# Kernel optimization log

Hardware: AMD Instinct MI355X
Metric: run time of the kernel (lower is better)

## Reference

```python
import jax, jax.numpy as jnp
import numpy as np

B, PIX_H, PIX_W = 64, 14, 14
ENC_D, DEC_D, ATT_D, EMB_D = 2048, 512, 512, 512
VOCAB, MAX_LEN = 10000, 52  # 51 decode steps


def setup_inputs() -> dict:
    key = jax.random.key(0)
    ks = jax.random.split(key, 24)
    s = 0.02
    inp = {
        'encoder_out': jax.random.normal(ks[0], (B, PIX_H, PIX_W, ENC_D), jnp.float32),
        'encoded_captions': jax.random.randint(ks[1], (B, MAX_LEN), 0, VOCAB),
        'caption_lengths': jnp.sort(jax.random.randint(ks[2], (B,), 2, MAX_LEN + 1))[::-1].at[0].set(MAX_LEN),
        # embedding (uniform -0.1..0.1 as in init_weights)
        'emb': jax.random.uniform(ks[3], (VOCAB, EMB_D), jnp.float32, -0.1, 0.1),
        # attention network
        'W_enc_att': jax.random.normal(ks[4], (ENC_D, ATT_D)) * s,
        'b_enc_att': jnp.zeros((ATT_D,)),
        'W_dec_att': jax.random.normal(ks[5], (DEC_D, ATT_D)) * s,
        'b_dec_att': jnp.zeros((ATT_D,)),
        'W_full_att': jax.random.normal(ks[6], (ATT_D, 1)) * s,
        'b_full_att': jnp.zeros((1,)),
        # init hidden state
        'W_init_h': jax.random.normal(ks[7], (ENC_D, DEC_D)) * s,
        'b_init_h': jnp.zeros((DEC_D,)),
        'W_init_c': jax.random.normal(ks[8], (ENC_D, DEC_D)) * s,
        'b_init_c': jnp.zeros((DEC_D,)),
        # gate
        'W_fbeta': jax.random.normal(ks[9], (DEC_D, ENC_D)) * s,
        'b_fbeta': jnp.zeros((ENC_D,)),
        # LSTMCell (torch gate order i,f,g,o)
        'W_ih': jax.random.normal(ks[10], (EMB_D + ENC_D, 4 * DEC_D)) * s,
        'W_hh': jax.random.normal(ks[11], (DEC_D, 4 * DEC_D)) * s,
        'b_ih': jnp.zeros((4 * DEC_D,)),
        'b_hh': jnp.zeros((4 * DEC_D,)),
        # fc (uniform -0.1..0.1, zero bias per init_weights)
        'W_fc': jax.random.uniform(ks[12], (DEC_D, VOCAB), jnp.float32, -0.1, 0.1),
        'b_fc': jnp.zeros((VOCAB,)),
    }
    return inp


def _decode(encoder_out, encoded_captions, caption_lengths, emb,
            W_enc_att, b_enc_att, W_dec_att, b_dec_att, W_full_att, b_full_att,
            W_init_h, b_init_h, W_init_c, b_init_c, W_fbeta, b_fbeta,
            W_ih, W_hh, b_ih, b_hh, W_fc, b_fc):
    bsz = encoder_out.shape[0]
    enc = encoder_out.reshape(bsz, -1, encoder_out.shape[-1])  # [B, P, ENC_D]
    embeddings = emb[encoded_captions]                          # [B, T+1, E]
    mean_enc = enc.mean(axis=1)
    h0 = mean_enc @ W_init_h + b_init_h
    c0 = mean_enc @ W_init_c + b_init_c
    att_enc = enc @ W_enc_att + b_enc_att                       # [B, P, A] precomputed
    T = encoded_captions.shape[1] - 1                           # max decode steps
    decode_len = caption_lengths - 1                            # [B]
    step_mask = jnp.arange(T)[:, None] < decode_len[None, :]    # [T, B]
    emb_seq = jnp.swapaxes(embeddings[:, :T, :], 0, 1)          # [T, B, E]

    def step(carry, xt):
        h, c = carry
        emb_t, m = xt                                           # [B,E], [B]
        # attention: 2 linears + tanh + softmax + weighted sum
        att_dec = h @ W_dec_att + b_dec_att                     # [B, A]
        e = (jnp.tanh(att_enc + att_dec[:, None, :]) @ W_full_att + b_full_att)[..., 0]  # [B, P]
        alpha = jax.nn.softmax(e, axis=-1)
        awe = jnp.einsum('bp,bpd->bd', alpha, enc)              # [B, ENC_D]
        gate = jax.nn.sigmoid(h @ W_fbeta + b_fbeta)
        awe = gate * awe
        # LSTMCell
        x = jnp.concatenate([emb_t, awe], axis=1)
        gates = x @ W_ih + h @ W_hh + (b_ih + b_hh)
        i, f, g, o = jnp.split(gates, 4, axis=1)
        c_new = jax.nn.sigmoid(f) * c + jax.nn.sigmoid(i) * jnp.tanh(g)
        h_new = jax.nn.sigmoid(o) * jnp.tanh(c_new)
        mm = m[:, None]
        h = jnp.where(mm, h_new, h)  # freeze finished rows (== batch_size_t slicing)
        c = jnp.where(mm, c_new, c)
        preds = (h @ W_fc + b_fc) * mm  # dropout = identity (eval mode)
        return (h, c), (preds, alpha * mm)

    (_, _), (preds_seq, alpha_seq) = jax.lax.scan(step, (h0, c0), (emb_seq, step_mask))
    predictions = jnp.swapaxes(preds_seq, 0, 1)  # [B, T, V]
    alphas = jnp.swapaxes(alpha_seq, 0, 1)       # [B, T, P]
    return predictions, alphas


def reference(encoder_out, encoded_captions, caption_lengths, emb,
              W_enc_att, b_enc_att, W_dec_att, b_dec_att, W_full_att, b_full_att,
              W_init_h, b_init_h, W_init_c, b_init_c, W_fbeta, b_fbeta,
              W_ih, W_hh, b_ih, b_hh, W_fc, b_fc):
    predictions, alphas = _decode(encoder_out, encoded_captions, caption_lengths, emb,
                                  W_enc_att, b_enc_att, W_dec_att, b_dec_att, W_full_att, b_full_att,
                                  W_init_h, b_init_h, W_init_c, b_init_c, W_fbeta, b_fbeta,
                                  W_ih, W_hh, b_ih, b_hh, W_fc, b_fc)
    return predictions, encoded_captions, caption_lengths - 1, alphas
```

## Files before the change

kernel.cpp:

```cpp
#include <hip/hip_runtime.h>
#include <hip/hip_bf16.h>
#include <math.h>

#define BB 64
#define NPIX 196
#define ENCD 2048
#define DECD 512
#define VOCAB_N 10000
#define MAXLEN 52
#define TT 51
#define NPADFC 10048

#define PRED_SZ   (BB * TT * VOCAB_N)
#define CAPS_SZ   (BB * MAXLEN)
#define LENS_SZ   (BB)
#define ALPHAS_OFF (PRED_SZ + CAPS_SZ + LENS_SZ)

typedef __attribute__((ext_vector_type(8))) short short8;
typedef __attribute__((ext_vector_type(4))) short short4v;
typedef __attribute__((ext_vector_type(4))) float f32x4;

__device__ __forceinline__ float fsigm(float x) {
    return 1.0f / (1.0f + __expf(-x));
}
__device__ __forceinline__ float ftanh(float x) {
    x = fminf(fmaxf(x, -15.0f), 15.0f);
    float e = __expf(2.0f * x);
    return (e - 1.0f) / (e + 1.0f);
}
__device__ __forceinline__ float bf2f(unsigned short u) {
    union { unsigned int i; float f; } v;
    v.i = ((unsigned int)u) << 16;
    return v.f;
}
__device__ __forceinline__ unsigned short f2bf(float f) {
    union { float f; unsigned int i; } v;
    v.f = f;
    unsigned int r = v.i + 0x7FFFu + ((v.i >> 16) & 1u);
    return (unsigned short)(r >> 16);
}

__global__ __launch_bounds__(256) void gemm_mfma(
    const unsigned short* __restrict__ A, int lda,
    const unsigned short* __restrict__ Wp, int Npad,
    int nkb, long slice_stride,
    float* __restrict__ C, unsigned short* __restrict__ C16, long ldc,
    const float* __restrict__ bias, int N, int act,
    const int* __restrict__ caplen, int t)
{
    const int n0 = blockIdx.x * 64;
    const int m0 = blockIdx.y * 64;
    const int kz = blockIdx.z;
    A  += (size_t)kz * nkb * 32;
    Wp += (size_t)kz * nkb * Npad * 32;
    if (C) C += (size_t)kz * slice_stride;

    const int w  = threadIdx.x >> 6;
    const int l  = threadIdx.x & 63;
    const int lr = l & 15;
    const int q  = l >> 4;

    const unsigned short* ap = A + (size_t)(m0 + 16 * w + lr) * lda + q * 8;
    const unsigned short* bp = Wp + (size_t)(n0 + lr) * 32 + q * 8;
    const size_t bstep = (size_t)Npad * 32;

    f32x4 acc[4];
#pragma unroll
    for (int i = 0; i < 4; ++i) acc[i] = (f32x4){0.f, 0.f, 0.f, 0.f};

    short8 a  = *(const short8*)ap;
    short8 b0 = *(const short8*)(bp);
    short8 b1 = *(const short8*)(bp + 512);
    short8 b2 = *(const short8*)(bp + 1024);
    short8 b3 = *(const short8*)(bp + 1536);

    for (int kb = 0; kb < nkb; ++kb) {
        const size_t nxt = (kb + 1 < nkb) ? 1 : 0;
        const unsigned short* apn = ap + nxt * 32;
        const unsigned short* bpn = bp + nxt * bstep;
        short8 an  = *(const short8*)apn;
        short8 bn0 = *(const short8*)(bpn);
        short8 bn1 = *(const short8*)(bpn + 512);
        short8 bn2 = *(const short8*)(bpn + 1024);
        short8 bn3 = *(const short8*)(bpn + 1536);
        acc[0] = __builtin_amdgcn_mfma_f32_16x16x32_bf16(a, b0, acc[0], 0, 0, 0);
        acc[1] = __builtin_amdgcn_mfma_f32_16x16x32_bf16(a, b1, acc[1], 0, 0, 0);
        acc[2] = __builtin_amdgcn_mfma_f32_16x16x32_bf16(a, b2, acc[2], 0, 0, 0);
        acc[3] = __builtin_amdgcn_mfma_f32_16x16x32_bf16(a, b3, acc[3], 0, 0, 0);
        a = an; b0 = bn0; b1 = bn1; b2 = bn2; b3 = bn3;
        ap = apn; bp = bpn;
    }

    const int r0 = q * 4;
#pragma unroll
    for (int cf = 0; cf < 4; ++cf) {
        int col = n0 + cf * 16 + lr;
        if (col >= N) continue;
        float bv = bias ? bias[col] : 0.f;
#pragma unroll
        for (int r = 0; r < 4; ++r) {
            int row = m0 + 16 * w + r0 + r;
            float v = acc[cf][r] + bv;
            if (act == 1 || (act == 2 && col < 2048)) v = fsigm(v);
            if (caplen) v *= (t < caplen[row] - 1) ? 1.f : 0.f;
            if (C16) C16[(size_t)row * ldc + col] = f2bf(v);
            else     C [(size_t)row * ldc + col] = v;
        }
    }
}

__global__ __launch_bounds__(256) void gateslstm_kernel(
    const unsigned short* __restrict__ xcatEG,
    const unsigned short* __restrict__ hprev,
    const unsigned short* __restrict__ WpLi,
    const float* __restrict__ bsum,
    const int* __restrict__ caplen, int t,
    float* __restrict__ c,
    unsigned short* __restrict__ hnext)
{
    __shared__ float gt[4][16][68];

    const int bx = blockIdx.x;
    const int nx = bx & 31;
    const int my = bx >> 5;
    const int m0 = my * 16;
    const int n0 = nx * 64;
    const int tid = threadIdx.x;
    const int ws = tid >> 6;
    const int l  = tid & 63;
    const int lr = l & 15;
    const int q  = l >> 4;

    const unsigned short* arow_x = xcatEG + (size_t)(m0 + lr) * 2560;
    const unsigned short* arow_h = hprev  + (size_t)(m0 + lr) * 512;
    const int kbase = ws * 768 + q * 8;

    const unsigned short* bp = WpLi + ((size_t)(ws * 24) * 2048 + n0 + lr) * 32 + q * 8;
    const size_t bstep = (size_t)2048 * 32;

    f32x4 acc[4];
#pragma unroll
    for (int i = 0; i < 4; ++i) acc[i] = (f32x4){0.f, 0.f, 0.f, 0.f};

#define ALOAD(kb) ({ int k0_ = kbase + (kb) * 32; \
    (k0_ < 2560) ? *(const short8*)(arow_x + k0_) \
                 : *(const short8*)(arow_h + (k0_ - 2560)); })

    short8 a  = ALOAD(0);
    short8 b0 = *(const short8*)(bp);
    short8 b1 = *(const short8*)(bp + 512);
    short8 b2 = *(const short8*)(bp + 1024);
    short8 b3 = *(const short8*)(bp + 1536);

    for (int kb = 0; kb < 24; ++kb) {
        const int kn = (kb + 1 < 24) ? kb + 1 : kb;
        const unsigned short* bpn = bp + ((kb + 1 < 24) ? bstep : 0);
        short8 an  = ALOAD(kn);
        short8 bn0 = *(const short8*)(bpn);
        short8 bn1 = *(const short8*)(bpn + 512);
        short8 bn2 = *(const short8*)(bpn + 1024);
        short8 bn3 = *(const short8*)(bpn + 1536);
        acc[0] = __builtin_amdgcn_mfma_f32_16x16x32_bf16(a, b0, acc[0], 0, 0, 0);
        acc[1] = __builtin_amdgcn_mfma_f32_16x16x32_bf16(a, b1, acc[1], 0, 0, 0);
        acc[2] = __builtin_amdgcn_mfma_f32_16x16x32_bf16(a, b2, acc[2], 0, 0, 0);
        acc[3] = __builtin_amdgcn_mfma_f32_16x16x32_bf16(a, b3, acc[3], 0, 0, 0);
        a = an; b0 = bn0; b1 = bn1; b2 = bn2; b3 = bn3;
        bp = bpn;
    }
#undef ALOAD

    const int r0 = q * 4;
#pragma unroll
    for (int cf = 0; cf < 4; ++cf)
#pragma unroll
        for (int r = 0; r < 4; ++r)
            gt[ws][r0 + r][cf * 16 + lr] = acc[cf][r];
    __syncthreads();

    const int row = tid & 15;
    const int jj  = tid >> 4;
    const int b   = m0 + row;
    const int j   = nx * 16 + jj;
    const int lc  = 4 * jj;
    float gi = bsum[j],        gf = bsum[512 + j];
    float gg = bsum[1024 + j], go = bsum[1536 + j];
#pragma unroll
    for (int s = 0; s < 4; ++s) {
        gi += gt[s][row][lc + 0];
        gf += gt[s][row][lc + 1];
        gg += gt[s][row][lc + 2];
        go += gt[s][row][lc + 3];
    }
    const int cidx = b * 512 + j;
    float cn = fsigm(gf) * c[cidx] + fsigm(gi) * ftanh(gg);
    float hn = fsigm(go) * ftanh(cn);
    bool upd = (t < caplen[b] - 1);
    if (upd) c[cidx] = cn;
    hnext[cidx] = upd ? f2bf(hn) : hprev[cidx];
}

__global__ __launch_bounds__(512) void attawe_kernel(
    const float* __restrict__ gadec,
    const unsigned short* __restrict__ attenc16,
    const unsigned short* __restrict__ enc16,
    const float* __restrict__ Wf, const float* __restrict__ bf_,
    const float* __restrict__ emb, const int* __restrict__ caps,
    const int* __restrict__ caplen, int t,
    unsigned short* __restrict__ xcatEG,
    float* __restrict__ alphas_out)
{
    int b  = blockIdx.x & 63;
    int dh = blockIdx.x >> 6;
    int tid = threadIdx.x;
    int lane = tid & 63, wid = tid >> 6;
    __shared__ float av[512];
    __shared__ float wv[512];
    __shared__ float es[NPIX];
    __shared__ float alpha_s[NPIX];
    __shared__ float r8[8];
    __shared__ float smax, ssum;

    av[tid] = gadec[(size_t)b * 2560 + 2048 + tid];
    wv[tid] = Wf[tid];
    __syncthreads();

    float mya[8], myw[8];
#pragma unroll
    for (int i = 0; i < 8; ++i) {
        mya[i] = av[lane * 8 + i];
        myw[i] = wv[lane * 8 + i];
    }

    float bf0 = bf_[0];
    for (int p = wid; p < NPIX; p += 8) {
        const unsigned short* ae = attenc16 + ((size_t)(b * NPIX + p)) * 512 + lane * 8;
        short8 e8 = *(const short8*)ae;
        float s = 0.f;
#pragma unroll
        for (int i = 0; i < 8; ++i)
            s += ftanh(bf2f((unsigned short)e8[i]) + mya[i]) * myw[i];
        for (int off = 32; off; off >>= 1) s += __shfl_down(s, off);
        if (lane == 0) es[p] = s + bf0;
    }
    __syncthreads();

    float v = (tid < NPIX) ? es[tid] : -1e30f;
    float m = v;
    for (int off = 32; off; off >>= 1) m = fmaxf(m, __shfl_down(m, off));
    if (lane == 0) r8[wid] = m;
    __syncthreads();
    if (tid == 0) {
        float mm = r8[0];
#pragma unroll
        for (int i = 1; i < 8; ++i) mm = fmaxf(mm, r8[i]);
        smax = mm;
    }
    __syncthreads();

    float ev = (tid < NPIX) ? __expf(v - smax) : 0.0f;
    float s = ev;
    for (int off = 32; off; off >>= 1) s += __shfl_down(s, off);
    if (lane == 0) r8[wid] = s;
    __syncthreads();
    if (tid == 0) {
        float ss = 0.f;
#pragma unroll
        for (int i = 0; i < 8; ++i) ss += r8[i];
        ssum = ss;
    }
    __syncthreads();

    float mk = (t < caplen[b] - 1) ? 1.0f : 0.0f;
    if (tid < NPIX) {
        float a = ev / ssum;
        alpha_s[tid] = a;
        if (dh == 0)
            alphas_out[((size_t)b * TT + t) * NPIX + tid] = a * mk;
    }
    __syncthreads();

    unsigned short* xr = xcatEG + (size_t)b * 2560;
    int d0 = dh * 1024 + tid * 2;
    const unsigned short* e = enc16 + (size_t)b * NPIX * ENCD + d0;
    float s0 = 0.f, s1 = 0.f;
    for (int p = 0; p < NPIX; ++p) {
        unsigned int vv = *(const unsigned int*)(e + (size_t)p * ENCD);
        float a = alpha_s[p];
        s0 += a * bf2f((unsigned short)(vv & 0xffffu));
        s1 += a * bf2f((unsigned short)(vv >> 16));
    }
    const float* gtt = gadec + (size_t)b * 2560 + d0;
    xr[512 + d0 + 0] = f2bf(s0 * gtt[0]);
    xr[512 + d0 + 1] = f2bf(s1 * gtt[1]);

    if (dh == 0) {
        int wword = caps[b * MAXLEN + t];
        xr[tid] = f2bf(emb[(size_t)wword * 512 + tid]);
    }
}

__global__ __launch_bounds__(256) void preds_gemm(
    const unsigned short* __restrict__ hhist,
    const unsigned short* __restrict__ WpF,
    const float* __restrict__ bfc,
    const int* __restrict__ caplen,
    float* __restrict__ out)
{
    if (blockIdx.x >= 157) return;
    const int n0 = blockIdx.x * 64;
    const int row0 = blockIdx.y * 64;
    const int w  = threadIdx.x >> 6;
    const int l  = threadIdx.x & 63;
    const int lr = l & 15;
    const int q  = l >> 4;

    const unsigned short* ap = hhist + (size_t)(row0 + 16 * w + lr) * 512 + q * 8;
    const unsigned short* bp = WpF + (size_t)(n0 + lr) * 32 + q * 8;
    const size_t bstep = (size_t)NPADFC * 32;

    f32x4 acc[4];
#pragma unroll
    for (int i = 0; i < 4; ++i) acc[i] = (f32x4){0.f, 0.f, 0.f, 0.f};

    short8 a  = *(const short8*)ap;
    short8 b0 = *(const short8*)(bp);
    short8 b1 = *(const short8*)(bp + 512);
    short8 b2 = *(const short8*)(bp + 1024);
    short8 b3 = *(const short8*)(bp + 1536);

    for (int kb = 0; kb < 16; ++kb) {
        const size_t nxt = (kb + 1 < 16) ? 1 : 0;
        const unsigned short* apn = ap + nxt * 32;
        const unsigned short* bpn = bp + nxt * bstep;
        short8 an  = *(const short8*)apn;
        short8 bn0 = *(const short8*)(bpn);
        short8 bn1 = *(const short8*)(bpn + 512);
        short8 bn2 = *(const short8*)(bpn + 1024);
        short8 bn3 = *(const short8*)(bpn + 1536);
        acc[0] = __builtin_amdgcn_mfma_f32_16x16x32_bf16(a, b0, acc[0], 0, 0, 0);
        acc[1] = __builtin_amdgcn_mfma_f32_16x16x32_bf16(a, b1, acc[1], 0, 0, 0);
        acc[2] = __builtin_amdgcn_mfma_f32_16x16x32_bf16(a, b2, acc[2], 0, 0, 0);
        acc[3] = __builtin_amdgcn_mfma_f32_16x16x32_bf16(a, b3, acc[3], 0, 0, 0);
        a = an; b0 = bn0; b1 = bn1; b2 = bn2; b3 = bn3;
        ap = apn; bp = bpn;
    }

    const int r0 = q * 4;
#pragma unroll
    for (int cf = 0; cf < 4; ++cf) {
        int col = n0 + cf * 16 + lr;
        if (col >= VOCAB_N) continue;
        float bv = bfc[col];
#pragma unroll
        for (int r = 0; r < 4; ++r) {
            int row = row0 + 16 * w + r0 + r;
            int tt = row >> 6, b = row & 63;
            float mk = (tt < caplen[b] - 1) ? 1.f : 0.f;
            out[((size_t)b * TT + tt) * VOCAB_N + col] = (acc[cf][r] + bv) * mk;
        }
    }
}

__global__ void pack_kernel(const float* __restrict__ W1, const float* __restrict__ W2,
                            int N1, int N2, int K1, int Npad, int mode,
                            unsigned short* __restrict__ Wp, int total)
{
    int idx = blockIdx.x * 256 + threadIdx.x;
    if (idx >= total) return;
    int kk = idx & 31;
    int r  = idx >> 5;
    int n  = r % Npad;
    int kb = r / Npad;
    int k  = kb * 32 + kk;
    float v = 0.f;
    if (mode == 0) {
        if (n < N1) v = W1[(size_t)k * N1 + n];
    } else if (mode == 1) {
        v = (n < N1) ? W1[(size_t)k * N1 + n] : W2[(size_t)k * N2 + (n - N1)];
    } else {
        v = (k < K1) ? W1[(size_t)k * N1 + n] : W2[(size_t)(k - K1) * N1 + n];
    }
    Wp[idx] = f2bf(v);
}

__global__ void packGi_kernel(const float* __restrict__ Wih,
                              const float* __restrict__ Whh,
                              unsigned short* __restrict__ Wp, int total)
{
    int idx = blockIdx.x * 256 + threadIdx.x;
    if (idx >= total) return;
    int kk = idx & 31;
    int r  = idx >> 5;
    int n  = r % 2048;
    int kb = r / 2048;
    int k  = kb * 32 + kk;
    int oc = (n & 3) * 512 + (n >> 2);
    float v = (k < 2560) ? Wih[(size_t)k * 2048 + oc]
                         : Whh[(size_t)(k - 2560) * 2048 + oc];
    Wp[idx] = f2bf(v);
}

__global__ void cast_kernel(const float* __restrict__ src,
                            unsigned short* __restrict__ dst, int n)
{
    int i = (blockIdx.x * 256 + threadIdx.x) * 4;
    if (i >= n) return;
    float4 v = *(const float4*)(src + i);
    dst[i]     = f2bf(v.x);
    dst[i + 1] = f2bf(v.y);
    dst[i + 2] = f2bf(v.z);
    dst[i + 3] = f2bf(v.w);
}

__global__ void bias_prep(const float* __restrict__ bfb, const float* __restrict__ bda,
                          const float* __restrict__ bih, const float* __restrict__ bhh,
                          float* __restrict__ bcat, float* __restrict__ bsum)
{
    int i = blockIdx.x * 256 + threadIdx.x;
    if (i < 2048) { bcat[i] = bfb[i]; bsum[i] = bih[i] + bhh[i]; }
    else if (i < 2560) bcat[i] = bda[i - 2048];
}

__global__ void mean_kernel(const float* __restrict__ enc, float* __restrict__ me)
{
    int d = blockIdx.x * 256 + threadIdx.x;
    int b = blockIdx.y;
    const float* p = enc + (size_t)b * NPIX * ENCD + d;
    float s = 0.0f;
    for (int q = 0; q < NPIX; ++q) s += p[(size_t)q * ENCD];
    me[b * ENCD + d] = s * (1.0f / 196.0f);
}

__global__ void inithc_kernel(const float* __restrict__ me,
                              const float* __restrict__ Wh, const float* __restrict__ bh,
                              const float* __restrict__ Wc, const float* __restrict__ bc,
                              unsigned short* __restrict__ hh0, float* __restrict__ c)
{
    int idx = blockIdx.x * 256 + threadIdx.x;
    int b = idx >> 9, j = idx & 511;
    const float* m = me + b * ENCD;
    float sh = bh[j], sc = bc[j];
    for (int k = 0; k < ENCD; ++k) {
        float mv = m[k];
        sh += mv * Wh[(size_t)k * DECD + j];
        sc += mv * Wc[(size_t)k * DECD + j];
    }
    hh0[idx] = f2bf(sh);
    c[idx] = sc;
}

__global__ void copy_misc(const int* __restrict__ caps, const int* __restrict__ lens,
                          float* __restrict__ out)
{
    int i = blockIdx.x * 256 + threadIdx.x;
    if (i < CAPS_SZ) out[PRED_SZ + i] = (float)caps[i];
    else if (i < CAPS_SZ + LENS_SZ) out[PRED_SZ + i] = (float)(lens[i - CAPS_SZ] - 1);
}

__global__ __launch_bounds__(256) void encatt_gemm(
    const unsigned short* __restrict__ A,
    const unsigned short* __restrict__ Wp,
    const float* __restrict__ bias,
    unsigned short* __restrict__ C16)
{
    const int n0 = blockIdx.x * 128;
    const int m0 = blockIdx.y * 128;
    const int w  = threadIdx.x >> 6;
    const int l  = threadIdx.x & 63;
    const int lr = l & 15;
    const int q  = l >> 4;

    const unsigned short* ap = A + (size_t)(m0 + 16 * w + lr) * 2048 + q * 8;
    const unsigned short* bp = Wp + (size_t)(n0 + lr) * 32 + q * 8;
    const size_t bstep = (size_t)512 * 32;

    f32x4 acc[16];
#pragma unroll
    for (int i = 0; i < 16; ++i) acc[i] = (f32x4){0.f, 0.f, 0.f, 0.f};

    short8 a0 = *(const short8*)(ap);
    short8 a1 = *(const short8*)(ap + 64 * 2048);
    short8 b[8];
#pragma unroll
    for (int nt = 0; nt < 8; ++nt) b[nt] = *(const short8*)(bp + nt * 512);

    for (int kb = 0; kb < 64; ++kb) {
        const size_t nxt = (kb + 1 < 64) ? 1 : 0;
        const unsigned short* apn = ap + nxt * 32;
        const unsigned short* bpn = bp + nxt * bstep;
        short8 an0 = *(const short8*)(apn);
        short8 an1 = *(const short8*)(apn + 64 * 2048);
        short8 bn[8];
#pragma unroll
        for (int nt = 0; nt < 8; ++nt) bn[nt] = *(const short8*)(bpn + nt * 512);
#pragma unroll
        for (int nt = 0; nt < 8; ++nt) {
            acc[nt]     = __builtin_amdgcn_mfma_f32_16x16x32_bf16(a0, b[nt], acc[nt], 0, 0, 0);
            acc[8 + nt] = __builtin_amdgcn_mfma_f32_16x16x32_bf16(a1, b[nt], acc[8 + nt], 0, 0, 0);
        }
        a0 = an0; a1 = an1;
#pragma unroll
        for (int nt = 0; nt < 8; ++nt) b[nt] = bn[nt];
        ap = apn; bp = bpn;
    }

    const int r0 = q * 4;
#pragma unroll
    for (int mt = 0; mt < 2; ++mt) {
#pragma unroll
        for (int nt = 0; nt < 8; ++nt) {
            int col = n0 + nt * 16 + lr;
            float bv = bias[col];
#pragma unroll
            for (int r = 0; r < 4; ++r) {
                int row = m0 + mt * 64 + 16 * w + r0 + r;
                C16[(size_t)row * 512 + col] = f2bf(acc[mt * 8 + nt][r] + bv);
            }
        }
    }
}

extern "C" void kernel_launch(void* const* d_in, const int* in_sizes, int n_in,
                              void* d_out, int out_size, void* d_ws, size_t ws_size,
                              hipStream_t stream)
{
    (void)in_sizes; (void)n_in; (void)out_size; (void)ws_size;
    const float* enc        = (const float*)d_in[0];
    const int*   caps       = (const int*)d_in[1];
    const int*   lens       = (const int*)d_in[2];
    const float* emb        = (const float*)d_in[3];
    const float* W_enc_att  = (const float*)d_in[4];
    const float* b_enc_att  = (const float*)d_in[5];
    const float* W_dec_att  = (const float*)d_in[6];
    const float* b_dec_att  = (const float*)d_in[7];
    const float* W_full_att = (const float*)d_in[8];
    const float* b_full_att = (const float*)d_in[9];
    const float* W_init_h   = (const float*)d_in[10];
    const float* b_init_h   = (const float*)d_in[11];
    const float* W_init_c   = (const float*)d_in[12];
    const float* b_init_c   = (const float*)d_in[13];
    const float* W_fbeta    = (const float*)d_in[14];
    const float* b_fbeta    = (const float*)d_in[15];
    const float* W_ih       = (const float*)d_in[16];
    const float* W_hh       = (const float*)d_in[17];
    const float* b_ih       = (const float*)d_in[18];
    const float* b_hh       = (const float*)d_in[19];
    const float* W_fc       = (const float*)d_in[20];
    const float* b_fc       = (const float*)d_in[21];
    float* out = (float*)d_out;

    char* p = (char*)d_ws;
    unsigned short* enc16   = (unsigned short*)p; p += (size_t)BB * NPIX * ENCD * 2;
    unsigned short* attenc16= (unsigned short*)p; p += (size_t)BB * NPIX * 512 * 2;
    unsigned short* WpLi    = (unsigned short*)p; p += (size_t)96 * 2048 * 32 * 2;
    unsigned short* WpG     = (unsigned short*)p; p += (size_t)16 * 2560 * 32 * 2;
    unsigned short* WpF     = (unsigned short*)p; p += (size_t)16 * NPADFC * 32 * 2;
    unsigned short* WpE     = (unsigned short*)p; p += (size_t)64 * 512 * 32 * 2;
    unsigned short* xcatEG  = (unsigned short*)p; p += (size_t)BB * 2560 * 2;
    unsigned short* hh      = (unsigned short*)p; p += (size_t)(TT + 1) * BB * 512 * 2;
    float* gadec  = (float*)p; p += (size_t)BB * 2560 * 4;
    float* c      = (float*)p; p += (size_t)BB * 512 * 4;
    float* me     = (float*)p; p += (size_t)BB * ENCD * 4;
    float* bcat   = (float*)p; p += 2560 * 4;
    float* bsum   = (float*)p; p += 2048 * 4;

    {
        int n = BB * NPIX * ENCD;
        cast_kernel<<<(n / 4 + 255) / 256, 256, 0, stream>>>(enc, enc16, n);
    }
    { int tot = 96 * 2048 * 32;
      packGi_kernel<<<(tot + 255) / 256, 256, 0, stream>>>(W_ih, W_hh, WpLi, tot); }
    { int tot = 16 * 2560 * 32;
      pack_kernel<<<(tot + 255) / 256, 256, 0, stream>>>(W_fbeta, W_dec_att, 2048, 512, 0, 2560, 1, WpG, tot); }
    { int tot = 16 * NPADFC * 32;
      pack_kernel<<<(tot + 255) / 256, 256, 0, stream>>>(W_fc, nullptr, VOCAB_N, 0, 0, NPADFC, 0, WpF, tot); }
    { int tot = 64 * 512 * 32;
      pack_kernel<<<(tot + 255) / 256, 256, 0, stream>>>(W_enc_att, nullptr, 512, 0, 0, 512, 0, WpE, tot); }
    bias_prep<<<10, 256, 0, stream>>>(b_fbeta, b_dec_att, b_ih, b_hh, bcat, bsum);
    mean_kernel<<<dim3(8, 64), 256, 0, stream>>>(enc, me);
    inithc_kernel<<<128, 256, 0, stream>>>(me, W_init_h, b_init_h, W_init_c, b_init_c, hh, c);
    encatt_gemm<<<dim3(4, 98), 256, 0, stream>>>(enc16, WpE, b_enc_att, attenc16);
    copy_misc<<<14, 256, 0, stream>>>(caps, lens, out);

    gemm_mfma<<<dim3(40, 1, 1), 256, 0, stream>>>(
        hh, 512, WpG, 2560, 16, 0, gadec, nullptr, 2560,
        bcat, 2560, 2, nullptr, 0);

    for (int t = 0; t < TT; ++t) {
        attawe_kernel<<<128, 512, 0, stream>>>(
            gadec, attenc16, enc16, W_full_att, b_full_att,
            emb, caps, lens, t, xcatEG, out + ALPHAS_OFF);
        gateslstm_kernel<<<128, 256, 0, stream>>>(
            xcatEG, hh + (size_t)t * BB * 512, WpLi, bsum, lens, t,
            c, hh + (size_t)(t + 1) * BB * 512);
        if (t + 1 < TT) {
            gemm_mfma<<<dim3(40, 1, 1), 256, 0, stream>>>(
                hh + (size_t)(t + 1) * BB * 512, 512, WpG, 2560, 16, 0,
                gadec, nullptr, 2560, bcat, 2560, 2, nullptr, 0);
        }
    }

    preds_gemm<<<dim3(160, TT), 256, 0, stream>>>(hh + (size_t)BB * 512, WpF, b_fc, lens, out);
}
```

Baseline: 3.285 ms.

## Fuse decoder-attention/gate projection into LSTM kernel via split-K partials; widen preds tiles

Removes the per-step gemm_mfma launch by having each gateslstm block compute a partial product of its 16 new h columns against the fbeta/dec_att weights, writing 32 K-slice partial buffers. attawe then sums the 32 partials plus bias and applies the sigmoid itself. This saves one launch per step but adds scalar FMA work, extra partial-buffer traffic and a 32-way reduction in attawe. Separately, preds_gemm now computes two 64-row tiles per block to reuse the B fragments.

```diff
diff --git a/kernel.cpp b/kernel.cpp
--- a/kernel.cpp
+++ b/kernel.cpp
@@ -114,11 +114,14 @@
     const unsigned short* __restrict__ hprev,
     const unsigned short* __restrict__ WpLi,
     const float* __restrict__ bsum,
+    const unsigned short* __restrict__ WgV,
     const int* __restrict__ caplen, int t,
     float* __restrict__ c,
-    unsigned short* __restrict__ hnext)
+    unsigned short* __restrict__ hnext,
+    float* __restrict__ pgad)
 {
     __shared__ float gt[4][16][68];
+    __shared__ float hsh[16][17];
 
     const int bx = blockIdx.x;
     const int nx = bx & 31;
@@ -196,11 +199,33 @@
     float hn = fsigm(go) * ftanh(cn);
     bool upd = (t < caplen[b] - 1);
     if (upd) c[cidx] = cn;
-    hnext[cidx] = upd ? f2bf(hn) : hprev[cidx];
+    unsigned short hv = upd ? f2bf(hn) : hprev[cidx];
+    hnext[cidx] = hv;
+    hsh[row][jj] = bf2f(hv);
+    __syncthreads();
+
+    const int j0 = nx * 16;
+    float* pg = pgad + (size_t)nx * 64 * 2560;
+#pragma unroll
+    for (int i = 0; i < 10; ++i) {
+        int col = tid + (i << 8);
+        float wv[16];
+#pragma unroll
+        for (int u = 0; u < 16; ++u)
+            wv[u] = bf2f(WgV[(size_t)(j0 + u) * 2560 + col]);
+#pragma unroll
+        for (int r = 0; r < 16; ++r) {
+            float s = 0.f;
+#pragma unroll
+            for (int u = 0; u < 16; ++u) s += hsh[r][u] * wv[u];
+            pg[(size_t)(m0 + r) * 2560 + col] = s;
+        }
+    }
 }
 
 __global__ __launch_bounds__(512) void attawe_kernel(
-    const float* __restrict__ gadec,
+    const float* __restrict__ pgad, int nsl,
+    const float* __restrict__ bfb, const float* __restrict__ bda,
     const unsigned short* __restrict__ attenc16,
     const unsigned short* __restrict__ enc16,
     const float* __restrict__ Wf, const float* __restrict__ bf_,
@@ -220,7 +245,12 @@
     __shared__ float r8[8];
     __shared__ float smax, ssum;
 
-    av[tid] = gadec[(size_t)b * 2560 + 2048 + tid];
+    {
+        float aa = bda[tid];
+        for (int s = 0; s < nsl; ++s)
+            aa += pgad[((size_t)s * 64 + b) * 2560 + 2048 + tid];
+        av[tid] = aa;
+    }
     wv[tid] = Wf[tid];
     __syncthreads();
 
@@ -289,9 +319,14 @@
         s0 += a * bf2f((unsigned short)(vv & 0xffffu));
         s1 += a * bf2f((unsigned short)(vv >> 16));
     }
-    const float* gtt = gadec + (size_t)b * 2560 + d0;
-    xr[512 + d0 + 0] = f2bf(s0 * gtt[0]);
-    xr[512 + d0 + 1] = f2bf(s1 * gtt[1]);
+    float g0 = bfb[d0], g1 = bfb[d0 + 1];
+    for (int sI = 0; sI < nsl; ++sI) {
+        const float* pg = pgad + ((size_t)sI * 64 + b) * 2560 + d0;
+        g0 += pg[0]; g1 += pg[1];
+    }
+    g0 = fsigm(g0); g1 = fsigm(g1);
+    xr[512 + d0 + 0] = f2bf(s0 * g0);
+    xr[512 + d0 + 1] = f2bf(s1 * g1);
 
     if (dh == 0) {
         int wword = caps[b * MAXLEN + t];
@@ -308,21 +343,27 @@
 {
     if (blockIdx.x >= 157) return;
     const int n0 = blockIdx.x * 64;
-    const int row0 = blockIdx.y * 64;
+    const int row0 = blockIdx.y * 128;
+    const bool two = (row0 + 128 <= TT * BB);
     const int w  = threadIdx.x >> 6;
     const int l  = threadIdx.x & 63;
     const int lr = l & 15;
     const int q  = l >> 4;
 
-    const unsigned short* ap = hhist + (size_t)(row0 + 16 * w + lr) * 512 + q * 8;
+    const unsigned short* ap0 = hhist + (size_t)(row0 + 16 * w + lr) * 512 + q * 8;
+    const unsigned short* ap1 = ap0 + (size_t)64 * 512;
     const unsigned short* bp = WpF + (size_t)(n0 + lr) * 32 + q * 8;
     const size_t bstep = (size_t)NPADFC * 32;
 
-    f32x4 acc[4];
-#pragma unroll
-    for (int i = 0; i < 4; ++i) acc[i] = (f32x4){0.f, 0.f, 0.f, 0.f};
-
-    short8 a  = *(const short8*)ap;
+    f32x4 acc[4], acc2[4];
+#pragma unroll
+    for (int i = 0; i < 4; ++i) {
+        acc[i]  = (f32x4){0.f, 0.f, 0.f, 0.f};
+        acc2[i] = (f32x4){0.f, 0.f, 0.f, 0.f};
+    }
+
+    short8 a0 = *(const short8*)ap0;
+    short8 a1 = two ? *(const short8*)ap1 : a0;
     short8 b0 = *(const short8*)(bp);
     short8 b1 = *(const short8*)(bp + 512);
     short8 b2 = *(const short8*)(bp + 1024);
@@ -330,19 +371,25 @@
 
     for (int kb = 0; kb < 16; ++kb) {
         const size_t nxt = (kb + 1 < 16) ? 1 : 0;
-        const unsigned short* apn = ap + nxt * 32;
+        const unsigned short* apn0 = ap0 + nxt * 32;
+        const unsigned short* apn1 = ap1 + nxt * 32;
         const unsigned short* bpn = bp + nxt * bstep;
-        short8 an  = *(const short8*)apn;
+        short8 an0 = *(const short8*)apn0;
+        short8 an1 = two ? *(const short8*)apn1 : an0;
         short8 bn0 = *(const short8*)(bpn);
         short8 bn1 = *(const short8*)(bpn + 512);
         short8 bn2 = *(const short8*)(bpn + 1024);
         short8 bn3 = *(const short8*)(bpn + 1536);
-        acc[0] = __builtin_amdgcn_mfma_f32_16x16x32_bf16(a, b0, acc[0], 0, 0, 0);
-        acc[1] = __builtin_amdgcn_mfma_f32_16x16x32_bf16(a, b1, acc[1], 0, 0, 0);
-        acc[2] = __builtin_amdgcn_mfma_f32_16x16x32_bf16(a, b2, acc[2], 0, 0, 0);
-        acc[3] = __builtin_amdgcn_mfma_f32_16x16x32_bf16(a, b3, acc[3], 0, 0, 0);
-        a = an; b0 = bn0; b1 = bn1; b2 = bn2; b3 = bn3;
-        ap = apn; bp = bpn;
+        acc[0]  = __builtin_amdgcn_mfma_f32_16x16x32_bf16(a0, b0, acc[0], 0, 0, 0);
+        acc[1]  = __builtin_amdgcn_mfma_f32_16x16x32_bf16(a0, b1, acc[1], 0, 0, 0);
+        acc[2]  = __builtin_amdgcn_mfma_f32_16x16x32_bf16(a0, b2, acc[2], 0, 0, 0);
+        acc[3]  = __builtin_amdgcn_mfma_f32_16x16x32_bf16(a0, b3, acc[3], 0, 0, 0);
+        acc2[0] = __builtin_amdgcn_mfma_f32_16x16x32_bf16(a1, b0, acc2[0], 0, 0, 0);
+        acc2[1] = __builtin_amdgcn_mfma_f32_16x16x32_bf16(a1, b1, acc2[1], 0, 0, 0);
+        acc2[2] = __builtin_amdgcn_mfma_f32_16x16x32_bf16(a1, b2, acc2[2], 0, 0, 0);
+        acc2[3] = __builtin_amdgcn_mfma_f32_16x16x32_bf16(a1, b3, acc2[3], 0, 0, 0);
+        a0 = an0; a1 = an1; b0 = bn0; b1 = bn1; b2 = bn2; b3 = bn3;
+        ap0 = apn0; ap1 = apn1; bp = bpn;
     }
 
     const int r0 = q * 4;
@@ -357,6 +404,12 @@
             int tt = row >> 6, b = row & 63;
             float mk = (tt < caplen[b] - 1) ? 1.f : 0.f;
             out[((size_t)b * TT + tt) * VOCAB_N + col] = (acc[cf][r] + bv) * mk;
+            if (two) {
+                int row2 = row + 64;
+                int tt2 = row2 >> 6, b2 = row2 & 63;
+                float mk2 = (tt2 < caplen[b2] - 1) ? 1.f : 0.f;
+                out[((size_t)b2 * TT + tt2) * VOCAB_N + col] = (acc2[cf][r] + bv) * mk2;
+            }
         }
     }
 }
@@ -400,6 +453,19 @@
     Wp[idx] = f2bf(v);
 }
 
+__global__ void packGV_kernel(const float* __restrict__ Wfb,
+                              const float* __restrict__ Wda,
+                              unsigned short* __restrict__ Wp, int total)
+{
+    int idx = blockIdx.x * 256 + threadIdx.x;
+    if (idx >= total) return;
+    int n = idx % 2560;
+    int k = idx / 2560;
+    float v = (n < 2048) ? Wfb[(size_t)k * 2048 + n]
+                         : Wda[(size_t)k * 512 + (n - 2048)];
+    Wp[idx] = f2bf(v);
+}
+
 __global__ void cast_kernel(const float* __restrict__ src,
                             unsigned short* __restrict__ dst, int n)
 {
@@ -412,13 +478,11 @@
     dst[i + 3] = f2bf(v.w);
 }
 
-__global__ void bias_prep(const float* __restrict__ bfb, const float* __restrict__ bda,
-                          const float* __restrict__ bih, const float* __restrict__ bhh,
-                          float* __restrict__ bcat, float* __restrict__ bsum)
+__global__ void bsum_prep(const float* __restrict__ bih, const float* __restrict__ bhh,
+                          float* __restrict__ bsum)
 {
     int i = blockIdx.x * 256 + threadIdx.x;
-    if (i < 2048) { bcat[i] = bfb[i]; bsum[i] = bih[i] + bhh[i]; }
-    else if (i < 2560) bcat[i] = bda[i - 2048];
+    if (i < 2048) bsum[i] = bih[i] + bhh[i];
 }
 
 __global__ void mean_kernel(const float* __restrict__ enc, float* __restrict__ me)
@@ -556,12 +620,12 @@
     unsigned short* WpG     = (unsigned short*)p; p += (size_t)16 * 2560 * 32 * 2;
     unsigned short* WpF     = (unsigned short*)p; p += (size_t)16 * NPADFC * 32 * 2;
     unsigned short* WpE     = (unsigned short*)p; p += (size_t)64 * 512 * 32 * 2;
+    unsigned short* WgV     = (unsigned short*)p; p += (size_t)512 * 2560 * 2;
     unsigned short* xcatEG  = (unsigned short*)p; p += (size_t)BB * 2560 * 2;
     unsigned short* hh      = (unsigned short*)p; p += (size_t)(TT + 1) * BB * 512 * 2;
-    float* gadec  = (float*)p; p += (size_t)BB * 2560 * 4;
+    float* pgad   = (float*)p; p += (size_t)32 * BB * 2560 * 4;
     float* c      = (float*)p; p += (size_t)BB * 512 * 4;
     float* me     = (float*)p; p += (size_t)BB * ENCD * 4;
-    float* bcat   = (float*)p; p += 2560 * 4;
     float* bsum   = (float*)p; p += 2048 * 4;
 
     {
@@ -576,29 +640,27 @@
       pack_kernel<<<(tot + 255) / 256, 256, 0, stream>>>(W_fc, nullptr, VOCAB_N, 0, 0, NPADFC, 0, WpF, tot); }
     { int tot = 64 * 512 * 32;
       pack_kernel<<<(tot + 255) / 256, 256, 0, stream>>>(W_enc_att, nullptr, 512, 0, 0, 512, 0, WpE, tot); }
-    bias_prep<<<10, 256, 0, stream>>>(b_fbeta, b_dec_att, b_ih, b_hh, bcat, bsum);
+    { int tot = 512 * 2560;
+      packGV_kernel<<<(tot + 255) / 256, 256, 0, stream>>>(W_fbeta, W_dec_att, WgV, tot); }
+    bsum_prep<<<8, 256, 0, stream>>>(b_ih, b_hh, bsum);
     mean_kernel<<<dim3(8, 64), 256, 0, stream>>>(enc, me);
     inithc_kernel<<<128, 256, 0, stream>>>(me, W_init_h, b_init_h, W_init_c, b_init_c, hh, c);
     encatt_gemm<<<dim3(4, 98), 256, 0, stream>>>(enc16, WpE, b_enc_att, attenc16);
     copy_misc<<<14, 256, 0, stream>>>(caps, lens, out);
 
     gemm_mfma<<<dim3(40, 1, 1), 256, 0, stream>>>(
-        hh, 512, WpG, 2560, 16, 0, gadec, nullptr, 2560,
-        bcat, 2560, 2, nullptr, 0);
+        hh, 512, WpG, 2560, 16, 0, pgad, nullptr, 2560,
+        nullptr, 2560, 0, nullptr, 0);
 
     for (int t = 0; t < TT; ++t) {
         attawe_kernel<<<128, 512, 0, stream>>>(
-            gadec, attenc16, enc16, W_full_att, b_full_att,
+            pgad, (t == 0) ? 1 : 32, b_fbeta, b_dec_att,
+            attenc16, enc16, W_full_att, b_full_att,
             emb, caps, lens, t, xcatEG, out + ALPHAS_OFF);
         gateslstm_kernel<<<128, 256, 0, stream>>>(
-            xcatEG, hh + (size_t)t * BB * 512, WpLi, bsum, lens, t,
-            c, hh + (size_t)(t + 1) * BB * 512);
-        if (t + 1 < TT) {
-            gemm_mfma<<<dim3(40, 1, 1), 256, 0, stream>>>(
-                hh + (size_t)(t + 1) * BB * 512, 512, WpG, 2560, 16, 0,
-                gadec, nullptr, 2560, bcat, 2560, 2, nullptr, 0);
-        }
-    }
-
-    preds_gemm<<<dim3(160, TT), 256, 0, stream>>>(hh + (size_t)BB * 512, WpF, b_fc, lens, out);
-}
+            xcatEG, hh + (size_t)t * BB * 512, WpLi, bsum, WgV, lens, t,
+            c, hh + (size_t)(t + 1) * BB * 512, pgad);
+    }
+
+    preds_gemm<<<dim3(160, 26), 256, 0, stream>>>(hh + (size_t)BB * 512, WpF, b_fc, lens, out);
+}
```

Measured after the change: 7.558 ms. 130% more time.

## Double row tile in preds GEMM and move init-state projection onto MFMA

Applied to the files above, without the earlier changes.

The prediction GEMM now computes 128 rows per block instead of 64, reusing each loaded W_fc fragment for two A tiles. The grid shrinks to 26 row blocks, and a guard handles the odd final tile. The scalar fp32 init_h/init_c projection is replaced by packing both weights into one bf16 matrix and running it through the existing MFMA GEMM, with the mean computed from the bf16 encoder copy. This cuts a slow serial-K setup kernel and weight re-reads, at the cost of bf16 precision in the initial state and more register pressure in preds_gemm.

```diff
diff --git a/kernel.cpp b/kernel.cpp
--- a/kernel.cpp
+++ b/kernel.cpp
@@ -308,21 +308,27 @@
 {
     if (blockIdx.x >= 157) return;
     const int n0 = blockIdx.x * 64;
-    const int row0 = blockIdx.y * 64;
+    const int row0 = blockIdx.y * 128;
+    const bool two = (row0 + 128 <= TT * BB);
     const int w  = threadIdx.x >> 6;
     const int l  = threadIdx.x & 63;
     const int lr = l & 15;
     const int q  = l >> 4;
 
-    const unsigned short* ap = hhist + (size_t)(row0 + 16 * w + lr) * 512 + q * 8;
+    const unsigned short* ap0 = hhist + (size_t)(row0 + 16 * w + lr) * 512 + q * 8;
+    const unsigned short* ap1 = ap0 + (size_t)64 * 512;
     const unsigned short* bp = WpF + (size_t)(n0 + lr) * 32 + q * 8;
     const size_t bstep = (size_t)NPADFC * 32;
 
-    f32x4 acc[4];
-#pragma unroll
-    for (int i = 0; i < 4; ++i) acc[i] = (f32x4){0.f, 0.f, 0.f, 0.f};
-
-    short8 a  = *(const short8*)ap;
+    f32x4 acc[4], acc2[4];
+#pragma unroll
+    for (int i = 0; i < 4; ++i) {
+        acc[i]  = (f32x4){0.f, 0.f, 0.f, 0.f};
+        acc2[i] = (f32x4){0.f, 0.f, 0.f, 0.f};
+    }
+
+    short8 a0 = *(const short8*)ap0;
+    short8 a1 = two ? *(const short8*)ap1 : a0;
     short8 b0 = *(const short8*)(bp);
     short8 b1 = *(const short8*)(bp + 512);
     short8 b2 = *(const short8*)(bp + 1024);
@@ -330,19 +336,25 @@
 
     for (int kb = 0; kb < 16; ++kb) {
         const size_t nxt = (kb + 1 < 16) ? 1 : 0;
-        const unsigned short* apn = ap + nxt * 32;
+        const unsigned short* apn0 = ap0 + nxt * 32;
+        const unsigned short* apn1 = ap1 + nxt * 32;
         const unsigned short* bpn = bp + nxt * bstep;
-        short8 an  = *(const short8*)apn;
+        short8 an0 = *(const short8*)apn0;
+        short8 an1 = two ? *(const short8*)apn1 : an0;
         short8 bn0 = *(const short8*)(bpn);
         short8 bn1 = *(const short8*)(bpn + 512);
         short8 bn2 = *(const short8*)(bpn + 1024);
         short8 bn3 = *(const short8*)(bpn + 1536);
-        acc[0] = __builtin_amdgcn_mfma_f32_16x16x32_bf16(a, b0, acc[0], 0, 0, 0);
-        acc[1] = __builtin_amdgcn_mfma_f32_16x16x32_bf16(a, b1, acc[1], 0, 0, 0);
-        acc[2] = __builtin_amdgcn_mfma_f32_16x16x32_bf16(a, b2, acc[2], 0, 0, 0);
-        acc[3] = __builtin_amdgcn_mfma_f32_16x16x32_bf16(a, b3, acc[3], 0, 0, 0);
-        a = an; b0 = bn0; b1 = bn1; b2 = bn2; b3 = bn3;
-        ap = apn; bp = bpn;
+        acc[0]  = __builtin_amdgcn_mfma_f32_16x16x32_bf16(a0, b0, acc[0], 0, 0, 0);
+        acc[1]  = __builtin_amdgcn_mfma_f32_16x16x32_bf16(a0, b1, acc[1], 0, 0, 0);
+        acc[2]  = __builtin_amdgcn_mfma_f32_16x16x32_bf16(a0, b2, acc[2], 0, 0, 0);
+        acc[3]  = __builtin_amdgcn_mfma_f32_16x16x32_bf16(a0, b3, acc[3], 0, 0, 0);
+        acc2[0] = __builtin_amdgcn_mfma_f32_16x16x32_bf16(a1, b0, acc2[0], 0, 0, 0);
+        acc2[1] = __builtin_amdgcn_mfma_f32_16x16x32_bf16(a1, b1, acc2[1], 0, 0, 0);
+        acc2[2] = __builtin_amdgcn_mfma_f32_16x16x32_bf16(a1, b2, acc2[2], 0, 0, 0);
+        acc2[3] = __builtin_amdgcn_mfma_f32_16x16x32_bf16(a1, b3, acc2[3], 0, 0, 0);
+        a0 = an0; a1 = an1; b0 = bn0; b1 = bn1; b2 = bn2; b3 = bn3;
+        ap0 = apn0; ap1 = apn1; bp = bpn;
     }
 
     const int r0 = q * 4;
@@ -357,6 +369,12 @@
             int tt = row >> 6, b = row & 63;
             float mk = (tt < caplen[b] - 1) ? 1.f : 0.f;
             out[((size_t)b * TT + tt) * VOCAB_N + col] = (acc[cf][r] + bv) * mk;
+            if (two) {
+                int row2 = row + 64;
+                int tt2 = row2 >> 6, b2 = row2 & 63;
+                float mk2 = (tt2 < caplen[b2] - 1) ? 1.f : 0.f;
+                out[((size_t)b2 * TT + tt2) * VOCAB_N + col] = (acc2[cf][r] + bv) * mk2;
+            }
         }
     }
 }
@@ -414,39 +432,35 @@
 
 __global__ void bias_prep(const float* __restrict__ bfb, const float* __restrict__ bda,
                           const float* __restrict__ bih, const float* __restrict__ bhh,
-                          float* __restrict__ bcat, float* __restrict__ bsum)
+                          const float* __restrict__ bh, const float* __restrict__ bc,
+                          float* __restrict__ bcat, float* __restrict__ bsum,
+                          float* __restrict__ bcatI)
 {
     int i = blockIdx.x * 256 + threadIdx.x;
     if (i < 2048) { bcat[i] = bfb[i]; bsum[i] = bih[i] + bhh[i]; }
     else if (i < 2560) bcat[i] = bda[i - 2048];
-}
-
-__global__ void mean_kernel(const float* __restrict__ enc, float* __restrict__ me)
+    else if (i < 3072) bcatI[i - 2560] = bh[i - 2560];
+    else if (i < 3584) bcatI[i - 2560] = bc[i - 3072];
+}
+
+__global__ void mean_kernel(const unsigned short* __restrict__ enc16,
+                            unsigned short* __restrict__ me16)
 {
     int d = blockIdx.x * 256 + threadIdx.x;
     int b = blockIdx.y;
-    const float* p = enc + (size_t)b * NPIX * ENCD + d;
+    const unsigned short* p = enc16 + (size_t)b * NPIX * ENCD + d;
     float s = 0.0f;
-    for (int q = 0; q < NPIX; ++q) s += p[(size_t)q * ENCD];
-    me[b * ENCD + d] = s * (1.0f / 196.0f);
-}
-
-__global__ void inithc_kernel(const float* __restrict__ me,
-                              const float* __restrict__ Wh, const float* __restrict__ bh,
-                              const float* __restrict__ Wc, const float* __restrict__ bc,
-                              unsigned short* __restrict__ hh0, float* __restrict__ c)
+    for (int q = 0; q < NPIX; ++q) s += bf2f(p[(size_t)q * ENCD]);
+    me16[b * ENCD + d] = f2bf(s * (1.0f / 196.0f));
+}
+
+__global__ void inithc_fin(const float* __restrict__ hc0,
+                           unsigned short* __restrict__ hh0, float* __restrict__ c)
 {
     int idx = blockIdx.x * 256 + threadIdx.x;
     int b = idx >> 9, j = idx & 511;
-    const float* m = me + b * ENCD;
-    float sh = bh[j], sc = bc[j];
-    for (int k = 0; k < ENCD; ++k) {
-        float mv = m[k];
-        sh += mv * Wh[(size_t)k * DECD + j];
-        sc += mv * Wc[(size_t)k * DECD + j];
-    }
-    hh0[idx] = f2bf(sh);
-    c[idx] = sc;
+    hh0[idx] = f2bf(hc0[(size_t)b * 1024 + j]);
+    c[idx] = hc0[(size_t)b * 1024 + 512 + j];
 }
 
 __global__ void copy_misc(const int* __restrict__ caps, const int* __restrict__ lens,
@@ -556,13 +570,16 @@
     unsigned short* WpG     = (unsigned short*)p; p += (size_t)16 * 2560 * 32 * 2;
     unsigned short* WpF     = (unsigned short*)p; p += (size_t)16 * NPADFC * 32 * 2;
     unsigned short* WpE     = (unsigned short*)p; p += (size_t)64 * 512 * 32 * 2;
+    unsigned short* WpI     = (unsigned short*)p; p += (size_t)64 * 1024 * 32 * 2;
     unsigned short* xcatEG  = (unsigned short*)p; p += (size_t)BB * 2560 * 2;
     unsigned short* hh      = (unsigned short*)p; p += (size_t)(TT + 1) * BB * 512 * 2;
+    unsigned short* me16    = (unsigned short*)p; p += (size_t)BB * ENCD * 2;
     float* gadec  = (float*)p; p += (size_t)BB * 2560 * 4;
+    float* hc0    = (float*)p; p += (size_t)BB * 1024 * 4;
     float* c      = (float*)p; p += (size_t)BB * 512 * 4;
-    float* me     = (float*)p; p += (size_t)BB * ENCD * 4;
     float* bcat   = (float*)p; p += 2560 * 4;
     float* bsum   = (float*)p; p += 2048 * 4;
+    float* bcatI  = (float*)p; p += 1024 * 4;
 
     {
         int n = BB * NPIX * ENCD;
@@ -576,9 +593,15 @@
       pack_kernel<<<(tot + 255) / 256, 256, 0, stream>>>(W_fc, nullptr, VOCAB_N, 0, 0, NPADFC, 0, WpF, tot); }
     { int tot = 64 * 512 * 32;
       pack_kernel<<<(tot + 255) / 256, 256, 0, stream>>>(W_enc_att, nullptr, 512, 0, 0, 512, 0, WpE, tot); }
-    bias_prep<<<10, 256, 0, stream>>>(b_fbeta, b_dec_att, b_ih, b_hh, bcat, bsum);
-    mean_kernel<<<dim3(8, 64), 256, 0, stream>>>(enc, me);
-    inithc_kernel<<<128, 256, 0, stream>>>(me, W_init_h, b_init_h, W_init_c, b_init_c, hh, c);
+    { int tot = 64 * 1024 * 32;
+      pack_kernel<<<(tot + 255) / 256, 256, 0, stream>>>(W_init_h, W_init_c, 512, 512, 0, 1024, 1, WpI, tot); }
+    bias_prep<<<14, 256, 0, stream>>>(b_fbeta, b_dec_att, b_ih, b_hh, b_init_h, b_init_c,
+                                      bcat, bsum, bcatI);
+    mean_kernel<<<dim3(8, 64), 256, 0, stream>>>(enc16, me16);
+    gemm_mfma<<<dim3(16, 1, 1), 256, 0, stream>>>(
+        me16, 2048, WpI, 1024, 64, 0, hc0, nullptr, 1024,
+        bcatI, 1024, 0, nullptr, 0);
+    inithc_fin<<<128, 256, 0, stream>>>(hc0, hh, c);
     encatt_gemm<<<dim3(4, 98), 256, 0, stream>>>(enc16, WpE, b_enc_att, attenc16);
     copy_misc<<<14, 256, 0, stream>>>(caps, lens, out);
 
@@ -600,5 +623,5 @@
         }
     }
 
-    preds_gemm<<<dim3(160, TT), 256, 0, stream>>>(hh + (size_t)BB * 512, WpF, b_fc, lens, out);
-}
+    preds_gemm<<<dim3(160, 26), 256, 0, stream>>>(hh + (size_t)BB * 512, WpF, b_fc, lens, out);
+}
```

New measurement: 3.130 ms. -4.7%, faster.
